# Kernel optimization log

Hardware: AMD Instinct MI355X
Metric: run time of the kernel (lower is better)

Reference implementation:

```python
import jax, jax.numpy as jnp
import numpy as np

LN_EPS = 1e-5
NEG_SLOPE = 0.2
INF = float((1 << 32) - 1)


def _ln(x, g, b):
    m = x.mean(-1, keepdims=True)
    v = ((x - m) ** 2).mean(-1, keepdims=True)
    return (x - m) * jax.lax.rsqrt(v + LN_EPS) * g + b


def setup_inputs() -> dict:
    B, M, NPG = 128, 256, 192      # graphs, max nodes per graph, actual nodes per graph
    N = B * NPG                    # 24576 total nodes
    E = N * 16                     # 393216 edges (avg degree 16)
    d, H, Od = 256, 4, 64          # input/attn dim, heads, per-head dim
    out_dim = 256
    key = jax.random.key(0)
    ks = jax.random.split(key, 24)
    s = 0.05
    p = lambda k, sh: jax.random.normal(k, sh, jnp.float32) * s

    node_feat = jax.random.normal(ks[0], (N, d), jnp.float32)
    edge_feat = jax.random.normal(ks[1], (E, d), jnp.float32)
    edge_index = jax.random.randint(ks[2], (2, E), 0, N)
    ptr = jnp.arange(B + 1, dtype=jnp.int32) * NPG
    row_valid = jnp.arange(M) < NPG
    attn_mask = jnp.broadcast_to(row_valid[None, :, None] & row_valid[None, None, :], (B, M, M))

    return dict(
        node_feat=node_feat, attn_mask=attn_mask, edge_feat=edge_feat,
        edge_index=edge_index, num_nodes=N, ptr=ptr,
        Wq=p(ks[3], (d, H * Od)), Wk=p(ks[4], (d, H * Od)), Wv=p(ks[5], (d, H * Od)),
        alphaQ=p(ks[6], (H, Od)), alphaK=p(ks[7], (H, Od)), attn_bias=p(ks[8], (H, Od)),
        gin_eps=jnp.zeros((), jnp.float32),
        gin_W1=p(ks[9], (d, 2 * d)), gin_b1=jnp.zeros((2 * d,), jnp.float32),
        gin_W2=p(ks[10], (2 * d, d)), gin_b2=jnp.zeros((d,), jnp.float32),
        ln1_g=jnp.ones((d,), jnp.float32), ln1_b=jnp.zeros((d,), jnp.float32),
        ln2_g=jnp.ones((d,), jnp.float32), ln2_b=jnp.zeros((d,), jnp.float32),
        ff_W1=p(ks[11], (2 * d, out_dim)), ff_b1=jnp.zeros((out_dim,), jnp.float32),
        ff_W2=p(ks[12], (out_dim, out_dim)), ff_b2=jnp.zeros((out_dim,), jnp.float32),
    )


def reference(node_feat, attn_mask, edge_feat, edge_index, num_nodes, ptr,
              Wq, Wk, Wv, alphaQ, alphaK, attn_bias,
              gin_eps, gin_W1, gin_b1, gin_W2, gin_b2,
              ln1_g, ln1_b, ln2_g, ln2_b,
              ff_W1, ff_b1, ff_W2, ff_b2):
    B, M = attn_mask.shape[:2]
    N, d = node_feat.shape
    H = alphaQ.shape[0]

    # graph -> dense batch layout (scatter by (graph, local position))
    node_ids = jnp.arange(N)
    batch_id = jnp.searchsorted(ptr, node_ids, side='right') - 1
    local = node_ids - ptr[batch_id]
    attn_input = jnp.zeros((B, M, d), node_feat.dtype).at[batch_id, local].set(node_feat)

    # GAT-style additive multi-head attention
    Qp = (attn_input @ Wq).reshape(B, M, H, -1)
    Kp = (attn_input @ Wk).reshape(B, M, H, -1)
    Vp = (attn_input @ Wv).reshape(B, M, H, -1)
    aQ = jnp.einsum('bmhd,hd->bmh', Qp, alphaQ)
    aK = jnp.einsum('bmhd,hd->bmh', Kp, alphaK)
    w = jax.nn.leaky_relu(aQ[:, :, None, :] + aK[:, None, :, :], NEG_SLOPE)  # [B,Q,K,H]
    w = jnp.where(attn_mask[..., None], w, -INF)
    w = jax.nn.softmax(w, axis=2)
    attn_out = (jnp.einsum('bqkh,bkhd->bqhd', w, Vp) + attn_bias).reshape(B, M, -1)

    attn_res = _ln(attn_out + attn_input, ln1_g, ln1_b)[batch_id, local]  # back to [N, d]

    # GIN conv: relu(x[dst] + e) scatter-summed to src, then 2-layer MLP
    msg = jax.nn.relu(node_feat[edge_index[1]] + edge_feat)
    agg = jax.ops.segment_sum(msg, edge_index[0], num_segments=num_nodes)
    h = (1.0 + gin_eps) * node_feat + agg
    gin = jax.nn.relu(h @ gin_W1 + gin_b1) @ gin_W2 + gin_b2
    gin_res = _ln(gin + node_feat, ln2_g, ln2_b)

    x = jnp.concatenate([gin_res, attn_res], axis=-1)  # [N, 2d]
    return jax.nn.relu(x @ ff_W1 + ff_b1) @ ff_W2 + ff_b2
```

## Files before the change

kernel.cpp:

```cpp
#include <hip/hip_runtime.h>

#define LN_EPS 1e-5f
#define NEG_SLOPE 0.2f

typedef __attribute__((ext_vector_type(8))) short short8;
typedef __attribute__((ext_vector_type(4))) float f32x4;

__device__ __forceinline__ unsigned short f2bf(float f) {
  union { float f; unsigned int u; } v;
  v.f = f;
  unsigned int r = v.u + 0x7fffu + ((v.u >> 16) & 1u);
  return (unsigned short)(r >> 16);
}
__device__ __forceinline__ float bf2f(unsigned short u) {
  union { unsigned int u; float f; } v;
  v.u = ((unsigned int)u) << 16;
  return v.f;
}

template <bool RELU, bool BIAS, bool OUTBF>
__device__ __forceinline__ void gemm_role(
    int t, char* smemc, const unsigned short* __restrict__ A,
    const unsigned short* __restrict__ Bt, const float* __restrict__ bias,
    void* __restrict__ Cv, int N, int K) {
  uint4* As = (uint4*)smemc;
  uint4* Bs = (uint4*)smemc + 512;
  const int tid = threadIdx.x;
  const int wid = tid >> 6, lane = tid & 63;
  const int nC = N >> 7;
  const int row0 = (t / nC) << 6;
  const int col0 = (t % nC) << 7;
  const int wr = wid >> 1, wc = wid & 1;
  const int fr = lane & 15, fq = lane >> 4;

  f32x4 acc[2][4];
#pragma unroll
  for (int m = 0; m < 2; ++m)
#pragma unroll
    for (int n = 0; n < 4; ++n) acc[m][n] = (f32x4){0.f, 0.f, 0.f, 0.f};

  for (int k0 = 0; k0 < K; k0 += 64) {
    __syncthreads();
#pragma unroll
    for (int c = 0; c < 2; ++c) {
      int idx = c * 256 + tid;
      int row = idx >> 3, slot = idx & 7;
      As[row * 8 + (slot ^ (row & 7))] =
          *(const uint4*)(A + (size_t)(row0 + row) * K + k0 + slot * 8);
    }
#pragma unroll
    for (int c = 0; c < 4; ++c) {
      int idx = c * 256 + tid;
      int row = idx >> 3, slot = idx & 7;
      Bs[row * 8 + (slot ^ (row & 7))] =
          *(const uint4*)(Bt + (size_t)(col0 + row) * K + k0 + slot * 8);
    }
    __syncthreads();
#pragma unroll
    for (int kk = 0; kk < 2; ++kk) {
      short8 af[2], bfr[4];
#pragma unroll
      for (int m = 0; m < 2; ++m) {
        int row = wr * 32 + m * 16 + fr;
        af[m] = *(const short8*)&As[row * 8 + ((kk * 4 + fq) ^ (row & 7))];
      }
#pragma unroll
      for (int n = 0; n < 4; ++n) {
        int col = wc * 64 + n * 16 + fr;
        bfr[n] = *(const short8*)&Bs[col * 8 + ((kk * 4 + fq) ^ (col & 7))];
      }
#pragma unroll
      for (int m = 0; m < 2; ++m)
#pragma unroll
        for (int n = 0; n < 4; ++n)
          acc[m][n] = __builtin_amdgcn_mfma_f32_16x16x32_bf16(af[m], bfr[n],
                                                              acc[m][n], 0, 0, 0);
    }
  }

#pragma unroll
  for (int n = 0; n < 4; ++n) {
    const int col = col0 + wc * 64 + n * 16 + fr;
    const float bv = BIAS ? bias[col] : 0.f;
#pragma unroll
    for (int m = 0; m < 2; ++m) {
#pragma unroll
      for (int r = 0; r < 4; ++r) {
        int row = row0 + wr * 32 + m * 16 + fq * 4 + r;
        float v = acc[m][n][r];
        if (BIAS) v += bv;
        if (RELU) v = fmaxf(v, 0.f);
        if (OUTBF)
          ((unsigned short*)Cv)[(size_t)row * N + col] = f2bf(v);
        else
          ((float*)Cv)[(size_t)row * N + col] = v;
      }
    }
  }
}

__device__ __forceinline__ void gather_role(
    int t, const float* __restrict__ node, const float* __restrict__ ef,
    const int2* __restrict__ edges, const int* __restrict__ ofs,
    const float* __restrict__ eps_p, unsigned short* __restrict__ agg16) {
  const int n = t * 4 + (threadIdx.x >> 6);
  const int lane = threadIdx.x & 63;
  const int s0 = ofs[n];
  const int s1 = ofs[n + 1];
  const float epl = 1.f + eps_p[0];
  const f32x4* nodev = (const f32x4*)node;
  const f32x4* efv = (const f32x4*)ef;
  f32x4 xv = nodev[(size_t)n * 64 + lane];
  float a0 = epl * xv.x, a1 = epl * xv.y, a2 = epl * xv.z, a3 = epl * xv.w;
  int j = s0;
  for (; j + 4 <= s1; j += 4) {
    int2 ed0 = edges[j], ed1 = edges[j + 1], ed2 = edges[j + 2],
         ed3 = edges[j + 3];
    f32x4 e0 = __builtin_nontemporal_load(&efv[(size_t)ed0.x * 64 + lane]);
    f32x4 e1 = __builtin_nontemporal_load(&efv[(size_t)ed1.x * 64 + lane]);
    f32x4 e2 = __builtin_nontemporal_load(&efv[(size_t)ed2.x * 64 + lane]);
    f32x4 e3 = __builtin_nontemporal_load(&efv[(size_t)ed3.x * 64 + lane]);
    f32x4 m0 = nodev[(size_t)ed0.y * 64 + lane];
    f32x4 m1 = nodev[(size_t)ed1.y * 64 + lane];
    f32x4 m2 = nodev[(size_t)ed2.y * 64 + lane];
    f32x4 m3 = nodev[(size_t)ed3.y * 64 + lane];
    a0 += fmaxf(e0.x + m0.x, 0.f) + fmaxf(e1.x + m1.x, 0.f) +
          fmaxf(e2.x + m2.x, 0.f) + fmaxf(e3.x + m3.x, 0.f);
    a1 += fmaxf(e0.y + m0.y, 0.f) + fmaxf(e1.y + m1.y, 0.f) +
          fmaxf(e2.y + m2.y, 0.f) + fmaxf(e3.y + m3.y, 0.f);
    a2 += fmaxf(e0.z + m0.z, 0.f) + fmaxf(e1.z + m1.z, 0.f) +
          fmaxf(e2.z + m2.z, 0.f) + fmaxf(e3.z + m3.z, 0.f);
    a3 += fmaxf(e0.w + m0.w, 0.f) + fmaxf(e1.w + m1.w, 0.f) +
          fmaxf(e2.w + m2.w, 0.f) + fmaxf(e3.w + m3.w, 0.f);
  }
  for (; j < s1; ++j) {
    int2 ed = edges[j];
    f32x4 ev = __builtin_nontemporal_load(&efv[(size_t)ed.x * 64 + lane]);
    f32x4 mv = nodev[(size_t)ed.y * 64 + lane];
    a0 += fmaxf(ev.x + mv.x, 0.f);
    a1 += fmaxf(ev.y + mv.y, 0.f);
    a2 += fmaxf(ev.z + mv.z, 0.f);
    a3 += fmaxf(ev.w + mv.w, 0.f);
  }
  ushort4 o;
  o.x = f2bf(a0);
  o.y = f2bf(a1);
  o.z = f2bf(a2);
  o.w = f2bf(a3);
  *(ushort4*)(agg16 + (size_t)n * 256 + lane * 4) = o;
}

__device__ __forceinline__ void attn_role(
    int t, char* smemc, const float* __restrict__ aQ,
    const float* __restrict__ aK, const unsigned short* __restrict__ Vp16,
    const float* __restrict__ attn_bias, const int* __restrict__ ptr,
    unsigned short* __restrict__ attn16) {
  unsigned short* Vt = (unsigned short*)smemc;
  float* aQs = (float*)(smemc + 24576);
  float* aKs = aQs + 192;
  float* sinv = aKs + 192;
  float* kmax_s = sinv + 192;
  const int b = t >> 2, h = t & 3;
  const int n0 = ptr[b];
  const int tid = threadIdx.x;
  const int wid = tid >> 6, lane = tid & 63;

  if (tid < 192) {
    aQs[tid] = aQ[(size_t)(n0 + tid) * 4 + h];
    aKs[tid] = aK[(size_t)(n0 + tid) * 4 + h];
  }
  for (int i = tid; i < 1536; i += 256) {
    int k = i >> 3, cc = (i & 7) << 3;
    short8 v = *(const short8*)(Vp16 + (size_t)(n0 + k) * 256 + h * 64 + cc);
    int ks = k >> 3, kr = k & 7;
#pragma unroll
    for (int jj = 0; jj < 8; ++jj) {
      int c = cc + jj;
      Vt[c * 192 + ((ks ^ (c & 7)) << 3) + kr] = (unsigned short)v[jj];
    }
  }
  __syncthreads();
  if (wid == 0) {
    float m3 = fmaxf(fmaxf(aKs[lane], aKs[lane + 64]), aKs[lane + 128]);
#pragma unroll
    for (int off = 32; off; off >>= 1) m3 = fmaxf(m3, __shfl_xor(m3, off));
    if (lane == 0) kmax_s[0] = m3;
  }
  __syncthreads();
  const float kmax = kmax_s[0];
  const int fr = lane & 15, fq = lane >> 4;
  const int qbase = wid * 48;

  float aq_m[3], mm[3];
#pragma unroll
  for (int m = 0; m < 3; ++m) {
    float aqv = aQs[qbase + m * 16 + fr];
    aq_m[m] = aqv;
    float tt = aqv + kmax;
    mm[m] = tt > 0.f ? tt : NEG_SLOPE * tt;
  }

  f32x4 acc[3][4];
#pragma unroll
  for (int m = 0; m < 3; ++m)
#pragma unroll
    for (int n = 0; n < 4; ++n) acc[m][n] = (f32x4){0.f, 0.f, 0.f, 0.f};
  float psum[3] = {0.f, 0.f, 0.f};

  for (int ks = 0; ks < 6; ++ks) {
    short8 bf[4];
#pragma unroll
    for (int n = 0; n < 4; ++n) {
      int c = n * 16 + fr;
      bf[n] = *(const short8*)&Vt[c * 192 + ((((ks << 2) + fq) ^ (c & 7)) << 3)];
    }
    float ak[8];
#pragma unroll
    for (int j = 0; j < 8; ++j) ak[j] = aKs[(ks << 5) + (fq << 3) + j];
#pragma unroll
    for (int m = 0; m < 3; ++m) {
      short8 af;
      float ps = 0.f;
#pragma unroll
      for (int j = 0; j < 8; ++j) {
        float x = aq_m[m] + ak[j];
        x = x > 0.f ? x : NEG_SLOPE * x;
        float p = __expf(x - mm[m]);
        ps += p;
        af[j] = (short)f2bf(p);
      }
      psum[m] += ps;
#pragma unroll
      for (int n = 0; n < 4; ++n)
        acc[m][n] =
            __builtin_amdgcn_mfma_f32_16x16x32_bf16(af, bf[n], acc[m][n], 0, 0, 0);
    }
  }

#pragma unroll
  for (int m = 0; m < 3; ++m) {
    psum[m] += __shfl_xor(psum[m], 16);
    psum[m] += __shfl_xor(psum[m], 32);
  }
  if (fq == 0) {
#pragma unroll
    for (int m = 0; m < 3; ++m) sinv[qbase + m * 16 + fr] = 1.f / psum[m];
  }
  __syncthreads();

#pragma unroll
  for (int m = 0; m < 3; ++m) {
#pragma unroll
    for (int n = 0; n < 4; ++n) {
      int col = n * 16 + fr;
      float bv = attn_bias[h * 64 + col];
#pragma unroll
      for (int r = 0; r < 4; ++r) {
        int q = qbase + m * 16 + fq * 4 + r;
        float v = acc[m][n][r] * sinv[q] + bv;
        attn16[(size_t)(n0 + q) * 256 + h * 64 + col] = f2bf(v);
      }
    }
  }
}

__device__ __forceinline__ void ln1_role(
    int t, const unsigned short* __restrict__ xin,
    const float* __restrict__ res, const float* __restrict__ g,
    const float* __restrict__ bt, unsigned short* __restrict__ out) {
  const int n = t * 4 + (threadIdx.x >> 6);
  const int lane = threadIdx.x & 63;
  ushort4 xv = *(const ushort4*)(xin + (size_t)n * 256 + lane * 4);
  float v0 = bf2f(xv.x), v1 = bf2f(xv.y), v2 = bf2f(xv.z), v3 = bf2f(xv.w);
  float4 rv = *(const float4*)(res + (size_t)n * 256 + lane * 4);
  v0 += rv.x;
  v1 += rv.y;
  v2 += rv.z;
  v3 += rv.w;
  float s = v0 + v1 + v2 + v3;
  float ss = v0 * v0 + v1 * v1 + v2 * v2 + v3 * v3;
#pragma unroll
  for (int off = 32; off; off >>= 1) {
    s += __shfl_xor(s, off);
    ss += __shfl_xor(ss, off);
  }
  const float mean = s * (1.f / 256.f);
  const float var = ss * (1.f / 256.f) - mean * mean;
  const float rs = rsqrtf(var + LN_EPS);
  float4 gv = *(const float4*)(g + lane * 4);
  float4 bv = *(const float4*)(bt + lane * 4);
  ushort4 o;
  o.x = f2bf((v0 - mean) * rs * gv.x + bv.x);
  o.y = f2bf((v1 - mean) * rs * gv.y + bv.y);
  o.z = f2bf((v2 - mean) * rs * gv.z + bv.z);
  o.w = f2bf((v3 - mean) * rs * gv.w + bv.w);
  *(ushort4*)(out + (size_t)n * 512 + 256 + lane * 4) = o;
}

__global__ __launch_bounds__(256) void k_fold(
    const float* __restrict__ Wq, const float* __restrict__ Wk,
    const float* __restrict__ alphaQ, const float* __restrict__ alphaK,
    float* __restrict__ wqa, float* __restrict__ wka, int* __restrict__ ideg,
    int Nn) {
  int t = threadIdx.x;
  for (int i = t; i < Nn; i += 256) ideg[i] = 0;
  for (int h = 0; h < 4; ++h) {
    float sq = 0.f, sk = 0.f;
    for (int od = 0; od < 64; ++od) {
      sq += Wq[t * 256 + h * 64 + od] * alphaQ[h * 64 + od];
      sk += Wk[t * 256 + h * 64 + od] * alphaK[h * 64 + od];
    }
    wqa[t * 4 + h] = sq;
    wka[t * 4 + h] = sk;
  }
}

__global__ __launch_bounds__(256) void k_mega(
    const float* __restrict__ Wv, const float* __restrict__ gW1,
    const float* __restrict__ gW2, const float* __restrict__ fW1,
    const float* __restrict__ fW2, unsigned short* __restrict__ wvt,
    unsigned short* __restrict__ w1t, unsigned short* __restrict__ w2t,
    unsigned short* __restrict__ fw1t, unsigned short* __restrict__ fw2t,
    const int* __restrict__ ei, int* __restrict__ ideg, int E,
    const float* __restrict__ node_feat, unsigned short* __restrict__ nf16,
    const float* __restrict__ wqa, const float* __restrict__ wka,
    float* __restrict__ aQ, float* __restrict__ aK) {
  const int bid = blockIdx.x;
  if (bid < 2048) {
    int i = bid * 256 + threadIdx.x;
    const float* src;
    unsigned short* dst;
    int K, N, base;
    if (i < 65536) {
      src = Wv; dst = wvt; K = 256; N = 256; base = 0;
    } else if (i < 196608) {
      src = gW1; dst = w1t; K = 256; N = 512; base = 65536;
    } else if (i < 327680) {
      src = gW2; dst = w2t; K = 512; N = 256; base = 196608;
    } else if (i < 458752) {
      src = fW1; dst = fw1t; K = 512; N = 256; base = 327680;
    } else {
      src = fW2; dst = fw2t; K = 256; N = 256; base = 458752;
    }
    int j = i - base;
    int n = j / K, k = j - n * K;
    dst[j] = f2bf(src[(size_t)k * N + n]);
    return;
  }
  if (bid < 3584) {
    int e = (bid - 2048) * 256 + threadIdx.x;
    if (e < E) atomicAdd(&ideg[ei[e]], 1);
    return;
  }
  const int n = (bid - 3584) * 4 + (threadIdx.x >> 6);
  const int lane = threadIdx.x & 63;
  f32x4 x = ((const f32x4*)node_feat)[(size_t)n * 64 + lane];
  ushort4 o;
  o.x = f2bf(x.x);
  o.y = f2bf(x.y);
  o.z = f2bf(x.z);
  o.w = f2bf(x.w);
  ((ushort4*)nf16)[(size_t)n * 64 + lane] = o;
  float sq[4], sk[4];
  const int d0 = lane * 4;
#pragma unroll
  for (int h = 0; h < 4; ++h) {
    sq[h] = x.x * wqa[(d0 + 0) * 4 + h] + x.y * wqa[(d0 + 1) * 4 + h] +
            x.z * wqa[(d0 + 2) * 4 + h] + x.w * wqa[(d0 + 3) * 4 + h];
    sk[h] = x.x * wka[(d0 + 0) * 4 + h] + x.y * wka[(d0 + 1) * 4 + h] +
            x.z * wka[(d0 + 2) * 4 + h] + x.w * wka[(d0 + 3) * 4 + h];
  }
#pragma unroll
  for (int off = 32; off; off >>= 1) {
#pragma unroll
    for (int h = 0; h < 4; ++h) {
      sq[h] += __shfl_xor(sq[h], off);
      sk[h] += __shfl_xor(sk[h], off);
    }
  }
  if (lane == 0) {
#pragma unroll
    for (int h = 0; h < 4; ++h) {
      aQ[(size_t)n * 4 + h] = sq[h];
      aK[(size_t)n * 4 + h] = sk[h];
    }
  }
}

__global__ __launch_bounds__(1024) void k_scan(const int* __restrict__ deg,
                                               int* __restrict__ ofs,
                                               int* __restrict__ cursor,
                                               int Nn) {
  __shared__ int part[1024];
  const int t = threadIdx.x;
  const int CH = (Nn + 1023) / 1024;
  const int base = t * CH;
  int s = 0;
  for (int i = 0; i < CH; ++i) s += (base + i < Nn) ? deg[base + i] : 0;
  part[t] = s;
  __syncthreads();
  for (int off = 1; off < 1024; off <<= 1) {
    int v = (t >= off) ? part[t - off] : 0;
    __syncthreads();
    part[t] += v;
    __syncthreads();
  }
  int o = (t == 0) ? 0 : part[t - 1];
  for (int i = 0; i < CH; ++i) {
    if (base + i < Nn) {
      ofs[base + i] = o;
      cursor[base + i] = o;
      o += deg[base + i];
    }
  }
  if (t == 1023) ofs[Nn] = part[1023];
}

__global__ __launch_bounds__(256) void k_scatter(const int* __restrict__ ei,
                                                 int* __restrict__ cursor,
                                                 int2* __restrict__ edges,
                                                 int E) {
  int e = blockIdx.x * 256 + threadIdx.x;
  if (e < E) {
    int src = ei[e];
    int dst = ei[E + e];
    int pos = atomicAdd(&cursor[src], 1);
    edges[pos] = make_int2(e, dst);
  }
}

__global__ __launch_bounds__(256) void k_gv(
    int nbV, const unsigned short* __restrict__ nf16,
    const unsigned short* __restrict__ wvt, unsigned short* __restrict__ vp16,
    const float* __restrict__ node, const float* __restrict__ ef,
    const int2* __restrict__ edges, const int* __restrict__ ofs,
    const float* __restrict__ eps_p, unsigned short* __restrict__ agg16) {
  __shared__ __align__(16) char smem[24576];
  if ((int)blockIdx.x < nbV)
    gemm_role<false, false, true>(blockIdx.x, smem, nf16, wvt, nullptr, vp16,
                                  256, 256);
  else
    gather_role(blockIdx.x - nbV, node, ef, edges, ofs, eps_p, agg16);
}

__global__ __launch_bounds__(256) void k_fa(
    int nbA, const float* __restrict__ aQ, const float* __restrict__ aK,
    const unsigned short* __restrict__ vp16,
    const float* __restrict__ attn_bias, const int* __restrict__ ptr,
    unsigned short* __restrict__ at16, const unsigned short* __restrict__ agg16,
    const unsigned short* __restrict__ w1t, const float* __restrict__ gin_b1,
    unsigned short* __restrict__ t1_16) {
  __shared__ __align__(16) char smem[26944];
  if ((int)blockIdx.x < nbA)
    attn_role(blockIdx.x, smem, aQ, aK, vp16, attn_bias, ptr, at16);
  else
    gemm_role<true, true, true>(blockIdx.x - nbA, smem, agg16, w1t, gin_b1,
                                t1_16, 512, 256);
}

__global__ __launch_bounds__(256) void k_f2l(
    int nbG, const unsigned short* __restrict__ t1_16,
    const unsigned short* __restrict__ w2t, const float* __restrict__ gin_b2,
    float* __restrict__ buf0, const unsigned short* __restrict__ at16,
    const float* __restrict__ node_feat, const float* __restrict__ g,
    const float* __restrict__ bt, unsigned short* __restrict__ x2_16) {
  __shared__ __align__(16) char smem[24576];
  if ((int)blockIdx.x < nbG)
    gemm_role<false, true, false>(blockIdx.x, smem, t1_16, w2t, gin_b2, buf0,
                                  256, 512);
  else
    ln1_role(blockIdx.x - nbG, at16, node_feat, g, bt, x2_16);
}

template <bool RELU, bool BIAS, bool OUTBF>
__global__ __launch_bounds__(256) void k_gemm(
    const unsigned short* __restrict__ A, const unsigned short* __restrict__ Bt,
    const float* __restrict__ bias, void* __restrict__ Cv, int N, int K) {
  __shared__ __align__(16) char smem[24576];
  gemm_role<RELU, BIAS, OUTBF>(blockIdx.x, smem, A, Bt, bias, Cv, N, K);
}

__global__ __launch_bounds__(64) void k_ln2(
    const float* __restrict__ xin, const float* __restrict__ res,
    const float* __restrict__ g, const float* __restrict__ bt,
    unsigned short* __restrict__ out) {
  const int n = blockIdx.x;
  const int lane = threadIdx.x;
  float4 xv = *(const float4*)(xin + (size_t)n * 256 + lane * 4);
  float4 rv = *(const float4*)(res + (size_t)n * 256 + lane * 4);
  float v0 = xv.x + rv.x, v1 = xv.y + rv.y, v2 = xv.z + rv.z, v3 = xv.w + rv.w;
  float s = v0 + v1 + v2 + v3;
  float ss = v0 * v0 + v1 * v1 + v2 * v2 + v3 * v3;
#pragma unroll
  for (int off = 32; off; off >>= 1) {
    s += __shfl_xor(s, off);
    ss += __shfl_xor(ss, off);
  }
  const float mean = s * (1.f / 256.f);
  const float var = ss * (1.f / 256.f) - mean * mean;
  const float rs = rsqrtf(var + LN_EPS);
  float4 gv = *(const float4*)(g + lane * 4);
  float4 bv = *(const float4*)(bt + lane * 4);
  ushort4 o;
  o.x = f2bf((v0 - mean) * rs * gv.x + bv.x);
  o.y = f2bf((v1 - mean) * rs * gv.y + bv.y);
  o.z = f2bf((v2 - mean) * rs * gv.z + bv.z);
  o.w = f2bf((v3 - mean) * rs * gv.w + bv.w);
  *(ushort4*)(out + (size_t)n * 512 + lane * 4) = o;
}

extern "C" void kernel_launch(void* const* d_in, const int* in_sizes, int n_in,
                              void* d_out, int out_size, void* d_ws,
                              size_t ws_size, hipStream_t stream) {
  const float* node_feat = (const float*)d_in[0];
  const float* edge_feat = (const float*)d_in[2];
  const int* edge_index = (const int*)d_in[3];
  const int* ptr = (const int*)d_in[5];
  const float* Wq = (const float*)d_in[6];
  const float* Wk = (const float*)d_in[7];
  const float* Wv = (const float*)d_in[8];
  const float* alphaQ = (const float*)d_in[9];
  const float* alphaK = (const float*)d_in[10];
  const float* attn_bias = (const float*)d_in[11];
  const float* gin_eps = (const float*)d_in[12];
  const float* gin_W1 = (const float*)d_in[13];
  const float* gin_b1 = (const float*)d_in[14];
  const float* gin_W2 = (const float*)d_in[15];
  const float* gin_b2 = (const float*)d_in[16];
  const float* ln1_g = (const float*)d_in[17];
  const float* ln1_b = (const float*)d_in[18];
  const float* ln2_g = (const float*)d_in[19];
  const float* ln2_b = (const float*)d_in[20];
  const float* ff_W1 = (const float*)d_in[21];
  const float* ff_b1 = (const float*)d_in[22];
  const float* ff_W2 = (const float*)d_in[23];
  const float* ff_b2 = (const float*)d_in[24];

  const int N = in_sizes[0] / 256;
  const int E = in_sizes[2] / 256;
  const int B = in_sizes[5] - 1;

  float* ws = (float*)d_ws;
  float* buf0 = ws;
  unsigned short* x2_16 = (unsigned short*)(buf0 + (size_t)N * 256);
  unsigned short* agg16 = x2_16 + (size_t)N * 512;
  unsigned short* t1_16 = agg16 + (size_t)N * 256;
  unsigned short* h1_16 = t1_16 + (size_t)N * 512;
  unsigned short* nf16 = h1_16 + (size_t)N * 256;
  unsigned short* vp16 = nf16 + (size_t)N * 256;
  unsigned short* at16 = vp16 + (size_t)N * 256;
  unsigned short* wvt = at16 + (size_t)N * 256;
  unsigned short* w1t = wvt + 65536;
  unsigned short* w2t = w1t + 131072;
  unsigned short* ffw1t = w2t + 131072;
  unsigned short* ffw2t = ffw1t + 131072;
  float* wqa = (float*)(ffw2t + 65536);
  float* wka = wqa + 1024;
  float* aQ = wka + 1024;
  float* aK = aQ + (size_t)N * 4;
  int* ideg = (int*)(aK + (size_t)N * 4);
  int* ofs = ideg + N;
  int* cursor = ofs + N + 2;
  int2* edges = (int2*)(cursor + N);
  size_t need = (size_t)N * 256 * 4 + (size_t)N * 2304 * 2 + 1100000 +
                (size_t)N * 8 * 4 + (size_t)N * 16 + (size_t)E * 8 + 8192;
  if (ws_size < need) return;

  const int degB = (E + 255) / 256;

  k_fold<<<1, 256, 0, stream>>>(Wq, Wk, alphaQ, alphaK, wqa, wka, ideg, N);
  k_mega<<<2048 + degB + N / 4, 256, 0, stream>>>(
      Wv, gin_W1, gin_W2, ff_W1, ff_W2, wvt, w1t, w2t, ffw1t, ffw2t,
      edge_index, ideg, E, node_feat, nf16, wqa, wka, aQ, aK);

  k_scan<<<1, 1024, 0, stream>>>(ideg, ofs, cursor, N);
  k_scatter<<<degB, 256, 0, stream>>>(edge_index, cursor, edges, E);

  const int nbV = (N / 64) * 2;
  k_gv<<<nbV + N / 4, 256, 0, stream>>>(nbV, nf16, wvt, vp16, node_feat,
                                        edge_feat, edges, ofs, gin_eps, agg16);

  const int nbA = B * 4;
  k_fa<<<nbA + (N / 64) * 4, 256, 0, stream>>>(nbA, aQ, aK, vp16, attn_bias,
                                               ptr, at16, agg16, w1t, gin_b1,
                                               t1_16);

  const int nbG = (N / 64) * 2;
  k_f2l<<<nbG + N / 4, 256, 0, stream>>>(nbG, t1_16, w2t, gin_b2, buf0, at16,
                                         node_feat, ln1_g, ln1_b, x2_16);

  k_ln2<<<N, 64, 0, stream>>>(buf0, node_feat, ln2_g, ln2_b, x2_16);
  k_gemm<true, true, true><<<(N / 64) * 2, 256, 0, stream>>>(x2_16, ffw1t,
                                                             ff_b1, h1_16, 256,
                                                             512);
  k_gemm<false, true, false><<<(N / 64) * 2, 256, 0, stream>>>(
      h1_16, ffw2t, ff_b2, d_out, 256, 256);
}
```

Baseline: 334.7 us.

## Fuse GIN second GEMM with LayerNorm2 and gather neighbors from bf16 features

```diff
diff --git a/kernel.cpp b/kernel.cpp
--- a/kernel.cpp
+++ b/kernel.cpp
@@ -100,9 +100,10 @@
 }
 
 __device__ __forceinline__ void gather_role(
-    int t, const float* __restrict__ node, const float* __restrict__ ef,
-    const int2* __restrict__ edges, const int* __restrict__ ofs,
-    const float* __restrict__ eps_p, unsigned short* __restrict__ agg16) {
+    int t, const float* __restrict__ node, const unsigned short* __restrict__ nf16,
+    const float* __restrict__ ef, const int2* __restrict__ edges,
+    const int* __restrict__ ofs, const float* __restrict__ eps_p,
+    unsigned short* __restrict__ agg16) {
   const int n = t * 4 + (threadIdx.x >> 6);
   const int lane = threadIdx.x & 63;
   const int s0 = ofs[n];
@@ -110,6 +111,7 @@
   const float epl = 1.f + eps_p[0];
   const f32x4* nodev = (const f32x4*)node;
   const f32x4* efv = (const f32x4*)ef;
+  const ushort4* nfv = (const ushort4*)nf16;
   f32x4 xv = nodev[(size_t)n * 64 + lane];
   float a0 = epl * xv.x, a1 = epl * xv.y, a2 = epl * xv.z, a3 = epl * xv.w;
   int j = s0;
@@ -120,27 +122,27 @@
     f32x4 e1 = __builtin_nontemporal_load(&efv[(size_t)ed1.x * 64 + lane]);
     f32x4 e2 = __builtin_nontemporal_load(&efv[(size_t)ed2.x * 64 + lane]);
     f32x4 e3 = __builtin_nontemporal_load(&efv[(size_t)ed3.x * 64 + lane]);
-    f32x4 m0 = nodev[(size_t)ed0.y * 64 + lane];
-    f32x4 m1 = nodev[(size_t)ed1.y * 64 + lane];
-    f32x4 m2 = nodev[(size_t)ed2.y * 64 + lane];
-    f32x4 m3 = nodev[(size_t)ed3.y * 64 + lane];
-    a0 += fmaxf(e0.x + m0.x, 0.f) + fmaxf(e1.x + m1.x, 0.f) +
-          fmaxf(e2.x + m2.x, 0.f) + fmaxf(e3.x + m3.x, 0.f);
-    a1 += fmaxf(e0.y + m0.y, 0.f) + fmaxf(e1.y + m1.y, 0.f) +
-          fmaxf(e2.y + m2.y, 0.f) + fmaxf(e3.y + m3.y, 0.f);
-    a2 += fmaxf(e0.z + m0.z, 0.f) + fmaxf(e1.z + m1.z, 0.f) +
-          fmaxf(e2.z + m2.z, 0.f) + fmaxf(e3.z + m3.z, 0.f);
-    a3 += fmaxf(e0.w + m0.w, 0.f) + fmaxf(e1.w + m1.w, 0.f) +
-          fmaxf(e2.w + m2.w, 0.f) + fmaxf(e3.w + m3.w, 0.f);
+    ushort4 m0 = nfv[(size_t)ed0.y * 64 + lane];
+    ushort4 m1 = nfv[(size_t)ed1.y * 64 + lane];
+    ushort4 m2 = nfv[(size_t)ed2.y * 64 + lane];
+    ushort4 m3 = nfv[(size_t)ed3.y * 64 + lane];
+    a0 += fmaxf(e0.x + bf2f(m0.x), 0.f) + fmaxf(e1.x + bf2f(m1.x), 0.f) +
+          fmaxf(e2.x + bf2f(m2.x), 0.f) + fmaxf(e3.x + bf2f(m3.x), 0.f);
+    a1 += fmaxf(e0.y + bf2f(m0.y), 0.f) + fmaxf(e1.y + bf2f(m1.y), 0.f) +
+          fmaxf(e2.y + bf2f(m2.y), 0.f) + fmaxf(e3.y + bf2f(m3.y), 0.f);
+    a2 += fmaxf(e0.z + bf2f(m0.z), 0.f) + fmaxf(e1.z + bf2f(m1.z), 0.f) +
+          fmaxf(e2.z + bf2f(m2.z), 0.f) + fmaxf(e3.z + bf2f(m3.z), 0.f);
+    a3 += fmaxf(e0.w + bf2f(m0.w), 0.f) + fmaxf(e1.w + bf2f(m1.w), 0.f) +
+          fmaxf(e2.w + bf2f(m2.w), 0.f) + fmaxf(e3.w + bf2f(m3.w), 0.f);
   }
   for (; j < s1; ++j) {
     int2 ed = edges[j];
     f32x4 ev = __builtin_nontemporal_load(&efv[(size_t)ed.x * 64 + lane]);
-    f32x4 mv = nodev[(size_t)ed.y * 64 + lane];
-    a0 += fmaxf(ev.x + mv.x, 0.f);
-    a1 += fmaxf(ev.y + mv.y, 0.f);
-    a2 += fmaxf(ev.z + mv.z, 0.f);
-    a3 += fmaxf(ev.w + mv.w, 0.f);
+    ushort4 mv = nfv[(size_t)ed.y * 64 + lane];
+    a0 += fmaxf(ev.x + bf2f(mv.x), 0.f);
+    a1 += fmaxf(ev.y + bf2f(mv.y), 0.f);
+    a2 += fmaxf(ev.z + bf2f(mv.z), 0.f);
+    a3 += fmaxf(ev.w + bf2f(mv.w), 0.f);
   }
   ushort4 o;
   o.x = f2bf(a0);
@@ -264,11 +266,135 @@
   }
 }
 
+__device__ __forceinline__ void fc2ln_role(
+    int t, char* smemc, const unsigned short* __restrict__ A,
+    const unsigned short* __restrict__ Bt, const float* __restrict__ b2,
+    const float* __restrict__ res, const float* __restrict__ g,
+    const float* __restrict__ bln, unsigned short* __restrict__ x2) {
+  uint4* As = (uint4*)smemc;
+  uint4* Bs = (uint4*)smemc + 512;
+  float2* part = (float2*)((uint4*)smemc + 2560);
+  const int tid = threadIdx.x;
+  const int wid = tid >> 6, lane = tid & 63;
+  const int row0 = t << 6;
+  const int wr = wid >> 2, wc = wid & 3;
+  const int fr = lane & 15, fq = lane >> 4;
+  const int K = 512;
+
+  f32x4 acc[2][4];
+#pragma unroll
+  for (int m = 0; m < 2; ++m)
+#pragma unroll
+    for (int n = 0; n < 4; ++n) acc[m][n] = (f32x4){0.f, 0.f, 0.f, 0.f};
+
+  for (int k0 = 0; k0 < K; k0 += 64) {
+    __syncthreads();
+    {
+      int row = tid >> 3, slot = tid & 7;
+      As[row * 8 + (slot ^ (row & 7))] =
+          *(const uint4*)(A + (size_t)(row0 + row) * K + k0 + slot * 8);
+    }
+#pragma unroll
+    for (int c = 0; c < 4; ++c) {
+      int idx = c * 512 + tid;
+      int row = idx >> 3, slot = idx & 7;
+      Bs[row * 8 + (slot ^ (row & 7))] =
+          *(const uint4*)(Bt + (size_t)row * K + k0 + slot * 8);
+    }
+    __syncthreads();
+#pragma unroll
+    for (int kk = 0; kk < 2; ++kk) {
+      short8 af[2], bfr[4];
+#pragma unroll
+      for (int m = 0; m < 2; ++m) {
+        int row = wr * 32 + m * 16 + fr;
+        af[m] = *(const short8*)&As[row * 8 + ((kk * 4 + fq) ^ (row & 7))];
+      }
+#pragma unroll
+      for (int n = 0; n < 4; ++n) {
+        int col = wc * 64 + n * 16 + fr;
+        bfr[n] = *(const short8*)&Bs[col * 8 + ((kk * 4 + fq) ^ (col & 7))];
+      }
+#pragma unroll
+      for (int m = 0; m < 2; ++m)
+#pragma unroll
+        for (int n = 0; n < 4; ++n)
+          acc[m][n] = __builtin_amdgcn_mfma_f32_16x16x32_bf16(af[m], bfr[n],
+                                                              acc[m][n], 0, 0, 0);
+    }
+  }
+
+  float psum[2][4], psq[2][4];
+#pragma unroll
+  for (int m = 0; m < 2; ++m)
+#pragma unroll
+    for (int r = 0; r < 4; ++r) {
+      psum[m][r] = 0.f;
+      psq[m][r] = 0.f;
+    }
+#pragma unroll
+  for (int n = 0; n < 4; ++n) {
+    const int col = wc * 64 + n * 16 + fr;
+    const float bv = b2[col];
+#pragma unroll
+    for (int m = 0; m < 2; ++m) {
+#pragma unroll
+      for (int r = 0; r < 4; ++r) {
+        int row = row0 + wr * 32 + m * 16 + fq * 4 + r;
+        float v = acc[m][n][r] + bv + res[(size_t)row * 256 + col];
+        acc[m][n][r] = v;
+        psum[m][r] += v;
+        psq[m][r] += v * v;
+      }
+    }
+  }
+#pragma unroll
+  for (int off = 1; off < 16; off <<= 1) {
+#pragma unroll
+    for (int m = 0; m < 2; ++m)
+#pragma unroll
+      for (int r = 0; r < 4; ++r) {
+        psum[m][r] += __shfl_xor(psum[m][r], off);
+        psq[m][r] += __shfl_xor(psq[m][r], off);
+      }
+  }
+  if (fr == 0) {
+#pragma unroll
+    for (int m = 0; m < 2; ++m)
+#pragma unroll
+      for (int r = 0; r < 4; ++r)
+        part[(wr * 32 + m * 16 + fq * 4 + r) * 4 + wc] =
+            make_float2(psum[m][r], psq[m][r]);
+  }
+  __syncthreads();
+
+#pragma unroll
+  for (int m = 0; m < 2; ++m) {
+#pragma unroll
+    for (int r = 0; r < 4; ++r) {
+      const int lr = wr * 32 + m * 16 + fq * 4 + r;
+      float2 p0 = part[lr * 4 + 0], p1 = part[lr * 4 + 1],
+             p2 = part[lr * 4 + 2], p3 = part[lr * 4 + 3];
+      const float mean = (p0.x + p1.x + p2.x + p3.x) * (1.f / 256.f);
+      const float var =
+          (p0.y + p1.y + p2.y + p3.y) * (1.f / 256.f) - mean * mean;
+      const float rs = rsqrtf(var + LN_EPS);
+      const int row = row0 + lr;
+#pragma unroll
+      for (int n = 0; n < 4; ++n) {
+        const int col = wc * 64 + n * 16 + fr;
+        float v = (acc[m][n][r] - mean) * rs * g[col] + bln[col];
+        x2[(size_t)row * 512 + col] = f2bf(v);
+      }
+    }
+  }
+}
+
 __device__ __forceinline__ void ln1_role(
     int t, const unsigned short* __restrict__ xin,
     const float* __restrict__ res, const float* __restrict__ g,
     const float* __restrict__ bt, unsigned short* __restrict__ out) {
-  const int n = t * 4 + (threadIdx.x >> 6);
+  const int n = t * 8 + (threadIdx.x >> 6);
   const int lane = threadIdx.x & 63;
   ushort4 xv = *(const ushort4*)(xin + (size_t)n * 256 + lane * 4);
   float v0 = bf2f(xv.x), v1 = bf2f(xv.y), v2 = bf2f(xv.z), v3 = bf2f(xv.w);
@@ -440,7 +566,7 @@
     gemm_role<false, false, true>(blockIdx.x, smem, nf16, wvt, nullptr, vp16,
                                   256, 256);
   else
-    gather_role(blockIdx.x - nbV, node, ef, edges, ofs, eps_p, agg16);
+    gather_role(blockIdx.x - nbV, node, nf16, ef, edges, ofs, eps_p, agg16);
 }
 
 __global__ __launch_bounds__(256) void k_fa(
@@ -458,18 +584,19 @@
                                 t1_16, 512, 256);
 }
 
-__global__ __launch_bounds__(256) void k_f2l(
+__global__ __launch_bounds__(512) void k_f2l(
     int nbG, const unsigned short* __restrict__ t1_16,
     const unsigned short* __restrict__ w2t, const float* __restrict__ gin_b2,
-    float* __restrict__ buf0, const unsigned short* __restrict__ at16,
-    const float* __restrict__ node_feat, const float* __restrict__ g,
-    const float* __restrict__ bt, unsigned short* __restrict__ x2_16) {
-  __shared__ __align__(16) char smem[24576];
+    const float* __restrict__ node_feat, const float* __restrict__ ln2_g,
+    const float* __restrict__ ln2_b, const unsigned short* __restrict__ at16,
+    const float* __restrict__ ln1_g, const float* __restrict__ ln1_b,
+    unsigned short* __restrict__ x2_16) {
+  __shared__ __align__(16) char smem[43520];
   if ((int)blockIdx.x < nbG)
-    gemm_role<false, true, false>(blockIdx.x, smem, t1_16, w2t, gin_b2, buf0,
-                                  256, 512);
+    fc2ln_role(blockIdx.x, smem, t1_16, w2t, gin_b2, node_feat, ln2_g, ln2_b,
+               x2_16);
   else
-    ln1_role(blockIdx.x - nbG, at16, node_feat, g, bt, x2_16);
+    ln1_role(blockIdx.x - nbG, at16, node_feat, ln1_g, ln1_b, x2_16);
 }
 
 template <bool RELU, bool BIAS, bool OUTBF>
@@ -478,35 +605,6 @@
     const float* __restrict__ bias, void* __restrict__ Cv, int N, int K) {
   __shared__ __align__(16) char smem[24576];
   gemm_role<RELU, BIAS, OUTBF>(blockIdx.x, smem, A, Bt, bias, Cv, N, K);
-}
-
-__global__ __launch_bounds__(64) void k_ln2(
-    const float* __restrict__ xin, const float* __restrict__ res,
-    const float* __restrict__ g, const float* __restrict__ bt,
-    unsigned short* __restrict__ out) {
-  const int n = blockIdx.x;
-  const int lane = threadIdx.x;
-  float4 xv = *(const float4*)(xin + (size_t)n * 256 + lane * 4);
-  float4 rv = *(const float4*)(res + (size_t)n * 256 + lane * 4);
-  float v0 = xv.x + rv.x, v1 = xv.y + rv.y, v2 = xv.z + rv.z, v3 = xv.w + rv.w;
-  float s = v0 + v1 + v2 + v3;
-  float ss = v0 * v0 + v1 * v1 + v2 * v2 + v3 * v3;
-#pragma unroll
-  for (int off = 32; off; off >>= 1) {
-    s += __shfl_xor(s, off);
-    ss += __shfl_xor(ss, off);
-  }
-  const float mean = s * (1.f / 256.f);
-  const float var = ss * (1.f / 256.f) - mean * mean;
-  const float rs = rsqrtf(var + LN_EPS);
-  float4 gv = *(const float4*)(g + lane * 4);
-  float4 bv = *(const float4*)(bt + lane * 4);
-  ushort4 o;
-  o.x = f2bf((v0 - mean) * rs * gv.x + bv.x);
-  o.y = f2bf((v1 - mean) * rs * gv.y + bv.y);
-  o.z = f2bf((v2 - mean) * rs * gv.z + bv.z);
-  o.w = f2bf((v3 - mean) * rs * gv.w + bv.w);
-  *(ushort4*)(out + (size_t)n * 512 + lane * 4) = o;
 }
 
 extern "C" void kernel_launch(void* const* d_in, const int* in_sizes, int n_in,
@@ -585,11 +683,11 @@
                                                ptr, at16, agg16, w1t, gin_b1,
                                                t1_16);
 
-  const int nbG = (N / 64) * 2;
-  k_f2l<<<nbG + N / 4, 256, 0, stream>>>(nbG, t1_16, w2t, gin_b2, buf0, at16,
-                                         node_feat, ln1_g, ln1_b, x2_16);
-
-  k_ln2<<<N, 64, 0, stream>>>(buf0, node_feat, ln2_g, ln2_b, x2_16);
+  const int nbG = N / 64;
+  k_f2l<<<nbG + N / 8, 512, 0, stream>>>(nbG, t1_16, w2t, gin_b2, node_feat,
+                                         ln2_g, ln2_b, at16, ln1_g, ln1_b,
+                                         x2_16);
+
   k_gemm<true, true, true><<<(N / 64) * 2, 256, 0, stream>>>(x2_16, ffw1t,
                                                              ff_b1, h1_16, 256,
                                                              512);
```

Result: faster. 306.6 us (-8.4%).
